# Kernel tuning notes

Hardware: AMD Instinct MI355X
Metric: run time of the kernel (lower is better)

Reference implementation:

```python
import jax, jax.numpy as jnp
import numpy as np

TEMPERATURE = 30.0
NUM_KERNELS = 4


def setup_inputs() -> dict:
    key = jax.random.key(0)
    ks = jax.random.split(key, 7)
    B, H, W, C = 32, 56, 56, 256
    F, KH, KW, K = 256, 3, 3, NUM_KERNELS
    hidden = C // 4  # attention_reduction_ratio = 4
    x = jax.random.normal(ks[0], (B, H, W, C), dtype=jnp.float32)
    # K parallel conv kernels (HWIO layout) and biases
    fan = KH * KW * C
    kernels = jax.random.normal(ks[1], (K, KH, KW, C, F), dtype=jnp.float32) / np.sqrt(fan)
    biases = jnp.zeros((K, F), dtype=jnp.float32)
    # attention MLP: GAP -> Dense(C//4, relu) -> Dense(K)
    w1 = jax.random.normal(ks[2], (C, hidden), dtype=jnp.float32) / np.sqrt(C)
    b1 = jnp.zeros((hidden,), dtype=jnp.float32)
    w2 = jax.random.normal(ks[3], (hidden, K), dtype=jnp.float32) / np.sqrt(hidden)
    b2 = jnp.zeros((K,), dtype=jnp.float32)
    return {"x": x, "kernels": kernels, "biases": biases,
            "w1": w1, "b1": b1, "w2": w2, "b2": b2}


def reference(x, kernels, biases, w1, b1, w2, b2):
    # Attention router: GAP -> Dense(relu) -> Dense(K) -> softmax(logits / tau)
    pooled = jnp.mean(x, axis=(1, 2))                       # [B, C]
    h = jax.nn.relu(pooled @ w1 + b1)                       # [B, C//4]
    logits = h @ w2 + b2                                    # [B, K]
    attn = jax.nn.softmax(logits / TEMPERATURE, axis=-1)    # [B, K]

    # K parallel conv branches (stride 1, SAME padding, dilation 1, groups 1)
    def conv_k(w, b):
        y = jax.lax.conv_general_dilated(
            x, w, window_strides=(1, 1), padding='SAME',
            dimension_numbers=('NHWC', 'HWIO', 'NHWC'))
        return y + b                                        # [B, H, W, F]

    ys = jax.vmap(conv_k)(kernels, biases)                  # [K, B, H, W, F]
    # per-sample weighted aggregation of branch outputs
    out = jnp.einsum('kbhwf,bk->bhwf', ys, attn)            # [B, H, W, F]
    return out
```

## Files before the change

kernel.cpp:

```cpp
#include <hip/hip_runtime.h>
#include <hip/hip_bf16.h>
#include <stdint.h>

typedef __bf16 bf16_t;
typedef __bf16 bf16x4 __attribute__((ext_vector_type(4)));
typedef __bf16 bf16x8 __attribute__((ext_vector_type(8)));
typedef float floatx4 __attribute__((ext_vector_type(4)));

#define B_ 32
#define HP 58
#define WP 66

#define XPAD_OFF   0u
#define WAGG_OFF   62717952u
#define POOLED_OFF 100466688u
#define ATTN_OFF   100499456u
#define BIASAGG_OFF 100499968u

__device__ __forceinline__ void async_copy16(const void* gsrc, void* ldst) {
  __builtin_amdgcn_global_load_lds(
      (const __attribute__((address_space(1))) unsigned int*)gsrc,
      (__attribute__((address_space(3))) unsigned int*)ldst, 16, 0, 0);
}

__global__ __launch_bounds__(256)
void pad_pool(const float* __restrict__ x, bf16_t* __restrict__ xpad,
              float* __restrict__ pooled) {
  const int hp = blockIdx.x;
  const int b  = blockIdx.y;
  const int t  = threadIdx.x;
  const int c4 = (t & 63) << 2;
  const int wq = t >> 6;
  const int h  = hp - 1;
  const bool hvalid = (h >= 0) && (h < 56);
  bf16_t* dst = xpad + ((size_t)(b * 58 + hp)) * (66 * 256);
  const float* srcrow = x + ((size_t)(b * 56 + (hvalid ? h : 0))) * (56 * 256);
  floatx4 sum = {0.f, 0.f, 0.f, 0.f};
  for (int wp = wq; wp < 66; wp += 4) {
    const int w = wp - 1;
    floatx4 v = {0.f, 0.f, 0.f, 0.f};
    if (hvalid && (unsigned)w < 56u) {
      v = *(const floatx4*)(srcrow + w * 256 + c4);
      sum += v;
    }
    bf16x4 r;
#pragma unroll
    for (int j = 0; j < 4; ++j) r[j] = (bf16_t)v[j];
    *(bf16x4*)(dst + wp * 256 + c4) = r;
  }
  __shared__ floatx4 red[4][64];
  red[wq][t & 63] = sum;
  __syncthreads();
  if (hvalid && t < 64) {
    floatx4 s = red[0][t] + red[1][t] + red[2][t] + red[3][t];
#pragma unroll
    for (int j = 0; j < 4; ++j) atomicAdd(&pooled[b * 256 + t * 4 + j], s[j]);
  }
}

__global__ __launch_bounds__(256)
void router(const float* __restrict__ pooled, const float* __restrict__ w1,
            const float* __restrict__ b1, const float* __restrict__ w2,
            const float* __restrict__ b2, const float* __restrict__ biases,
            float* __restrict__ attn, float* __restrict__ biasagg) {
  __shared__ float ps[8192];
  __shared__ float w1s[16384];
  __shared__ float hs[2048];
  __shared__ float lg[128];
  __shared__ float at[128];
  const int t = threadIdx.x;
  for (int i = t; i < 8192; i += 256) ps[i] = pooled[i] * (1.0f / 3136.0f);
  for (int i = t; i < 4096; i += 256)
    *(floatx4*)&w1s[i * 4] = *(const floatx4*)&w1[i * 4];
  __syncthreads();
  for (int task = t; task < 2048; task += 256) {
    const int b = task >> 6, j = task & 63;
    const float* pb = ps + b * 256;
    float s0 = 0.f, s1 = 0.f, s2 = 0.f, s3 = 0.f;
#pragma unroll 4
    for (int c = 0; c < 256; c += 4) {
      s0 += pb[c]     * w1s[c * 64 + j];
      s1 += pb[c + 1] * w1s[(c + 1) * 64 + j];
      s2 += pb[c + 2] * w1s[(c + 2) * 64 + j];
      s3 += pb[c + 3] * w1s[(c + 3) * 64 + j];
    }
    hs[task] = fmaxf((s0 + s1) + (s2 + s3) + b1[j], 0.f);
  }
  __syncthreads();
  if (t < 128) {
    int b = t >> 2, k = t & 3;
    float s = b2[k];
    const float* hb = hs + b * 64;
#pragma unroll 4
    for (int j = 0; j < 64; ++j) s += hb[j] * w2[j * 4 + k];
    lg[t] = s * (1.0f / 30.0f);
  }
  __syncthreads();
  if (t < 32) {
    int b = t;
    float z0 = lg[b*4], z1 = lg[b*4+1], z2 = lg[b*4+2], z3 = lg[b*4+3];
    float m = fmaxf(fmaxf(z0, z1), fmaxf(z2, z3));
    float e0 = expf(z0-m), e1 = expf(z1-m), e2 = expf(z2-m), e3 = expf(z3-m);
    float inv = 1.0f / (e0 + e1 + e2 + e3);
    at[b*4] = e0*inv; at[b*4+1] = e1*inv; at[b*4+2] = e2*inv; at[b*4+3] = e3*inv;
    attn[b*4] = at[b*4]; attn[b*4+1] = at[b*4+1];
    attn[b*4+2] = at[b*4+2]; attn[b*4+3] = at[b*4+3];
  }
  __syncthreads();
  for (int i = t; i < 8192; i += 256) {
    int b = i >> 8, f = i & 255;
    biasagg[i] = at[b*4]*biases[f] + at[b*4+1]*biases[256+f]
               + at[b*4+2]*biases[512+f] + at[b*4+3]*biases[768+f];
  }
}

__global__ __launch_bounds__(256)
void wagg_kernel(const float* __restrict__ kers, const float* __restrict__ attn,
                 bf16_t* __restrict__ wagg) {
  const int lid = blockIdx.x;
  const int xcd = lid & 7;
  const int sl  = lid >> 3;
  const int c8  = sl & 7;
  const int tap = sl >> 3;
  const int b0  = xcd << 2;
  const int t   = threadIdx.x;
  __shared__ bf16_t tile[4][32 * 260];

  float a[4][4];
#pragma unroll
  for (int i = 0; i < 4; ++i)
#pragma unroll
    for (int k = 0; k < 4; ++k) a[i][k] = attn[(b0 + i) * 4 + k];

  const float* k0 = kers + ((size_t)(0 * 9 + tap)) * 65536 + (size_t)(c8 * 32) * 256;
  const float* k1 = kers + ((size_t)(1 * 9 + tap)) * 65536 + (size_t)(c8 * 32) * 256;
  const float* k2 = kers + ((size_t)(2 * 9 + tap)) * 65536 + (size_t)(c8 * 32) * 256;
  const float* k3 = kers + ((size_t)(3 * 9 + tap)) * 65536 + (size_t)(c8 * 32) * 256;

  const int fq = t & 63;
  const int cl = t >> 6;
  const int f0 = fq * 4;
#pragma unroll
  for (int pass = 0; pass < 8; ++pass) {
    const int c_local = pass * 4 + cl;
    const size_t o = (size_t)c_local * 256 + f0;
    floatx4 v0 = *(const floatx4*)(k0 + o);
    floatx4 v1 = *(const floatx4*)(k1 + o);
    floatx4 v2 = *(const floatx4*)(k2 + o);
    floatx4 v3 = *(const floatx4*)(k3 + o);
#pragma unroll
    for (int i = 0; i < 4; ++i) {
      bf16x4 r;
#pragma unroll
      for (int j = 0; j < 4; ++j)
        r[j] = (bf16_t)(a[i][0] * v0[j] + a[i][1] * v1[j] + a[i][2] * v2[j] + a[i][3] * v3[j]);
      *(bf16x4*)&tile[i][c_local * 260 + f0] = r;
    }
  }
  __syncthreads();

#pragma unroll
  for (int i = 0; i < 4; ++i) {
    bf16_t* wt = wagg + ((size_t)((b0 + i) * 9 + tap)) * 65536 + c8 * 32;
#pragma unroll
    for (int pass = 0; pass < 4; ++pass) {
      const int gi = pass * 256 + t;
      const int f  = gi >> 2;
      const int cg = gi & 3;
      bf16x8 v;
#pragma unroll
      for (int jj = 0; jj < 8; ++jj) v[jj] = tile[i][(cg * 8 + jj) * 260 + f];
      *(bf16x8*)(wt + (size_t)f * 256 + cg * 8) = v;
    }
  }
}

#define PBUF_BYTES 40960
#define BBUF_BYTES 32768

__global__ __launch_bounds__(512, 2)
void conv_mfma(const bf16_t* __restrict__ xpad, const bf16_t* __restrict__ wagg,
               const float* __restrict__ biasagg, float* __restrict__ out) {
  __shared__ char lds[PBUF_BYTES + 3 * BBUF_BYTES];
  char* ldsP = lds;
  char* ldsB = lds + PBUF_BYTES;

  const int lid  = blockIdx.y * 14 + blockIdx.x;
  const int nid  = (lid & 7) * 56 + (lid >> 3);
  const int b    = nid / 14;
  const int tile = nid - b * 14;
  const int h0 = (tile >> 1) * 8;
  const int w0 = (tile & 1) * 28;

  const int tid  = threadIdx.x;
  const int lane = tid & 63;
  const int wv   = tid >> 6;
  const int mg   = wv >> 2;
  const int fs   = wv & 3;
  const int l15  = lane & 15;
  const int quad = lane >> 4;
  const int n0   = fs * 64;

  const char* xb = (const char*)xpad + (size_t)b * (HP * WP * 256 * 2);
  const char* wb = (const char*)wagg + (size_t)b * (9 * 256 * 256 * 2);

  int offs[7];
#pragma unroll
  for (int mi = 0; mi < 7; ++mi) {
    int m = mg * 112 + mi * 16 + l15;
    int ty = m / 28;
    int tx = m - ty * 28;
    offs[mi] = ty * 32 + tx;
  }
  int boff[4];
#pragma unroll
  for (int ni = 0; ni < 4; ++ni) {
    int f = n0 + ni * 16 + l15;
    boff[ni] = f * 128 + ((quad ^ (f & 7)) << 4);
  }
  int sb_off[4];
#pragma unroll
  for (int ii = 0; ii < 4; ++ii) {
    int i32 = wv * 4 + ii;
    int f = i32 * 8 + (lane >> 3);
    int gsrc = (lane & 7) ^ (f & 7);
    sb_off[ii] = f * 512 + gsrc * 16;
  }
  int sp_off[5];
#pragma unroll
  for (int ii = 0; ii < 5; ++ii) {
    int i40 = wv * 5 + ii;
    int p = i40 * 8 + (lane >> 3);
    int row = p >> 5, col = p & 31;
    int gsrc = (lane & 7) ^ (p & 7);
    sp_off[ii] = ((h0 + row) * WP + (w0 + col)) * 512 + gsrc * 16;
  }

  floatx4 acc[7][4];
#pragma unroll
  for (int mi = 0; mi < 7; ++mi)
#pragma unroll
    for (int ni = 0; ni < 4; ++ni) acc[mi][ni] = (floatx4){0.f, 0.f, 0.f, 0.f};

  auto stage_patch = [&](int cq) {
#pragma unroll
    for (int ii = 0; ii < 5; ++ii)
      async_copy16(xb + cq * 128 + sp_off[ii], ldsP + (wv * 5 + ii) * 1024);
  };
  auto stage_b = [&](int tap, int cq, int slot) {
    const char* wtb = wb + (size_t)tap * 131072 + cq * 128;
#pragma unroll
    for (int ii = 0; ii < 4; ++ii)
      async_copy16(wtb + sb_off[ii], ldsB + slot * BBUF_BYTES + (wv * 4 + ii) * 1024);
  };

  stage_patch(0);
  stage_b(0, 0, 0);

  bf16x8 aA[7], aB[7];
  int aoff[7];
  int slot = 0;

#pragma unroll 1
  for (int d = 0; d < 36; ++d) {
    const int cq  = d / 9;
    const int tap = d - cq * 9;
    const int s1 = (slot == 2) ? 0 : slot + 1;
    const bool last = (d == 35);

    if (!last) {
      const int nt = (tap == 8) ? 0 : tap + 1;
      const int nc = (tap == 8) ? cq + 1 : cq;
      stage_b(nt, nc, s1);
      asm volatile("s_waitcnt vmcnt(4)" ::: "memory");
    } else {
      asm volatile("s_waitcnt vmcnt(0)" ::: "memory");
    }
    __builtin_amdgcn_s_barrier();
    __builtin_amdgcn_sched_barrier(0);

    const char* bc = ldsB + slot * BBUF_BYTES;
    bf16x8 bv0 = *(const bf16x8*)(bc + boff[0]);
    bf16x8 bv1 = *(const bf16x8*)(bc + boff[1]);
    bf16x8 bv2 = *(const bf16x8*)(bc + boff[2]);
    bf16x8 bv3 = *(const bf16x8*)(bc + boff[3]);
    if (tap == 0) {
#pragma unroll
      for (int mi = 0; mi < 7; ++mi) {
        int p = offs[mi];
        aoff[mi] = (p << 7) + ((quad ^ (p & 7)) << 4);
        aA[mi] = *(const bf16x8*)(ldsP + aoff[mi]);
      }
    }
    __builtin_amdgcn_s_setprio(1);
#pragma unroll
    for (int mi = 0; mi < 7; ++mi) {
      acc[mi][0] = __builtin_amdgcn_mfma_f32_16x16x32_bf16(aA[mi], bv0, acc[mi][0], 0, 0, 0);
      acc[mi][1] = __builtin_amdgcn_mfma_f32_16x16x32_bf16(aA[mi], bv1, acc[mi][1], 0, 0, 0);
      acc[mi][2] = __builtin_amdgcn_mfma_f32_16x16x32_bf16(aA[mi], bv2, acc[mi][2], 0, 0, 0);
      acc[mi][3] = __builtin_amdgcn_mfma_f32_16x16x32_bf16(aA[mi], bv3, acc[mi][3], 0, 0, 0);
    }
    __builtin_amdgcn_s_setprio(0);

    bf16x8 cv0 = *(const bf16x8*)(bc + (boff[0] ^ 64));
    bf16x8 cv1 = *(const bf16x8*)(bc + (boff[1] ^ 64));
    bf16x8 cv2 = *(const bf16x8*)(bc + (boff[2] ^ 64));
    bf16x8 cv3 = *(const bf16x8*)(bc + (boff[3] ^ 64));
#pragma unroll
    for (int mi = 0; mi < 7; ++mi)
      aB[mi] = *(const bf16x8*)(ldsP + (aoff[mi] ^ 64));
    if (tap < 8) {
      const int ntapoff = ((tap + 1) / 3) * 32 + ((tap + 1) % 3);
#pragma unroll
      for (int mi = 0; mi < 7; ++mi) {
        int p = offs[mi] + ntapoff;
        aoff[mi] = (p << 7) + ((quad ^ (p & 7)) << 4);
        aA[mi] = *(const bf16x8*)(ldsP + aoff[mi]);
      }
    }
    __builtin_amdgcn_s_setprio(1);
#pragma unroll
    for (int mi = 0; mi < 7; ++mi) {
      acc[mi][0] = __builtin_amdgcn_mfma_f32_16x16x32_bf16(aB[mi], cv0, acc[mi][0], 0, 0, 0);
      acc[mi][1] = __builtin_amdgcn_mfma_f32_16x16x32_bf16(aB[mi], cv1, acc[mi][1], 0, 0, 0);
      acc[mi][2] = __builtin_amdgcn_mfma_f32_16x16x32_bf16(aB[mi], cv2, acc[mi][2], 0, 0, 0);
      acc[mi][3] = __builtin_amdgcn_mfma_f32_16x16x32_bf16(aB[mi], cv3, acc[mi][3], 0, 0, 0);
    }
    __builtin_amdgcn_s_setprio(0);

    if (tap == 8 && cq < 3) {
      __builtin_amdgcn_s_barrier();
      stage_patch(cq + 1);
    }
    slot = s1;
  }

  float bias[4];
#pragma unroll
  for (int ni = 0; ni < 4; ++ni) bias[ni] = biasagg[b * 256 + n0 + ni * 16 + l15];
  float* outb = out + (size_t)b * (56 * 56 * 256);
#pragma unroll
  for (int mi = 0; mi < 7; ++mi) {
#pragma unroll
    for (int rg = 0; rg < 4; ++rg) {
      int m = mg * 112 + mi * 16 + quad * 4 + rg;
      int ty = m / 28, tx = m - ty * 28;
      float* orow = outb + ((size_t)((h0 + ty) * 56) + (w0 + tx)) * 256 + n0 + l15;
#pragma unroll
      for (int ni = 0; ni < 4; ++ni) orow[ni * 16] = acc[mi][ni][rg] + bias[ni];
    }
  }
}

extern "C" void kernel_launch(void* const* d_in, const int* in_sizes, int n_in,
                              void* d_out, int out_size, void* d_ws, size_t ws_size,
                              hipStream_t stream) {
  const float* x      = (const float*)d_in[0];
  const float* kers   = (const float*)d_in[1];
  const float* biases = (const float*)d_in[2];
  const float* w1     = (const float*)d_in[3];
  const float* b1     = (const float*)d_in[4];
  const float* w2     = (const float*)d_in[5];
  const float* b2     = (const float*)d_in[6];
  float* outp = (float*)d_out;
  char* ws = (char*)d_ws;

  bf16_t* xpad   = (bf16_t*)(ws + XPAD_OFF);
  bf16_t* wagg   = (bf16_t*)(ws + WAGG_OFF);
  float* pooled  = (float*)(ws + POOLED_OFF);
  float* attn    = (float*)(ws + ATTN_OFF);
  float* biasagg = (float*)(ws + BIASAGG_OFF);

  hipMemsetAsync(pooled, 0, 32 * 256 * sizeof(float), stream);
  pad_pool<<<dim3(58, 32), 256, 0, stream>>>(x, xpad, pooled);
  router<<<1, 256, 0, stream>>>(pooled, w1, b1, w2, b2, biases, attn, biasagg);
  wagg_kernel<<<dim3(576), 256, 0, stream>>>(kers, attn, wagg);
  conv_mfma<<<dim3(14, 32), 512, 0, stream>>>(xpad, wagg, biasagg, outp);
}
```

Baseline: 361.8 us.

## Double-buffer input patch in LDS and move to two-slot weight pipeline

Gives the input patch its own two LDS buffers. The next channel quarter's patch is now prefetched early (at tap 0) instead of after a barrier at the end of each quarter, so the tap-8 to tap-0 transition no longer stalls on a fresh patch load. The weight ring drops from three slots to two, and each iteration ends with a full vmcnt(0) wait. A-fragment loads for the next step are issued across the loop boundary, and the second-half B and A fragment reads are hoisted ahead of the first MFMA group. The shallower weight prefetch and per-iteration full wait may expose more global-load latency in exchange for fewer patch stalls and one fewer barrier per quarter.

Measured after the change: 357.0 us. Within noise of the previous version (-1.3%).

```diff
diff --git a/kernel.cpp b/kernel.cpp
--- a/kernel.cpp
+++ b/kernel.cpp
@@ -181,9 +181,10 @@
 __global__ __launch_bounds__(512, 2)
 void conv_mfma(const bf16_t* __restrict__ xpad, const bf16_t* __restrict__ wagg,
                const float* __restrict__ biasagg, float* __restrict__ out) {
-  __shared__ char lds[PBUF_BYTES + 3 * BBUF_BYTES];
-  char* ldsP = lds;
-  char* ldsB = lds + PBUF_BYTES;
+  __shared__ char lds[2 * PBUF_BYTES + 2 * BBUF_BYTES];
+  char* ldsP0 = lds;
+  char* ldsP1 = lds + PBUF_BYTES;
+  char* ldsB  = lds + 2 * PBUF_BYTES;
 
   const int lid  = blockIdx.y * 14 + blockIdx.x;
   const int nid  = (lid & 7) * 56 + (lid >> 3);
@@ -242,10 +243,10 @@
 #pragma unroll
     for (int ni = 0; ni < 4; ++ni) acc[mi][ni] = (floatx4){0.f, 0.f, 0.f, 0.f};
 
-  auto stage_patch = [&](int cq) {
+  auto stage_patch = [&](int cq, char* pdst) {
 #pragma unroll
     for (int ii = 0; ii < 5; ++ii)
-      async_copy16(xb + cq * 128 + sp_off[ii], ldsP + (wv * 5 + ii) * 1024);
+      async_copy16(xb + cq * 128 + sp_off[ii], pdst + (wv * 5 + ii) * 1024);
   };
   auto stage_b = [&](int tap, int cq, int slot) {
     const char* wtb = wb + (size_t)tap * 131072 + cq * 128;
@@ -254,44 +255,52 @@
       async_copy16(wtb + sb_off[ii], ldsB + slot * BBUF_BYTES + (wv * 4 + ii) * 1024);
   };
 
-  stage_patch(0);
+  stage_patch(0, ldsP0);
   stage_b(0, 0, 0);
+  asm volatile("s_waitcnt vmcnt(0)" ::: "memory");
+  __builtin_amdgcn_s_barrier();
+  __builtin_amdgcn_sched_barrier(0);
 
   bf16x8 aA[7], aB[7];
   int aoff[7];
-  int slot = 0;
+#pragma unroll
+  for (int mi = 0; mi < 7; ++mi) {
+    int p = offs[mi];
+    aoff[mi] = (p << 7) + ((quad ^ (p & 7)) << 4);
+    aA[mi] = *(const bf16x8*)(ldsP0 + aoff[mi]);
+  }
 
 #pragma unroll 1
   for (int d = 0; d < 36; ++d) {
     const int cq  = d / 9;
     const int tap = d - cq * 9;
-    const int s1 = (slot == 2) ? 0 : slot + 1;
-    const bool last = (d == 35);
-
-    if (!last) {
+    const int cs  = cq & 1;
+    char* pbc = cs ? ldsP1 : ldsP0;
+    char* pbn = cs ? ldsP0 : ldsP1;
+    const char* bc = ldsB + (d & 1) * BBUF_BYTES;
+    const bool haveNext = (d < 35);
+
+    __builtin_amdgcn_s_barrier();
+    __builtin_amdgcn_sched_barrier(0);
+
+    if (haveNext) {
       const int nt = (tap == 8) ? 0 : tap + 1;
       const int nc = (tap == 8) ? cq + 1 : cq;
-      stage_b(nt, nc, s1);
-      asm volatile("s_waitcnt vmcnt(4)" ::: "memory");
-    } else {
-      asm volatile("s_waitcnt vmcnt(0)" ::: "memory");
-    }
-    __builtin_amdgcn_s_barrier();
-    __builtin_amdgcn_sched_barrier(0);
-
-    const char* bc = ldsB + slot * BBUF_BYTES;
+      stage_b(nt, nc, (d + 1) & 1);
+    }
+
     bf16x8 bv0 = *(const bf16x8*)(bc + boff[0]);
     bf16x8 bv1 = *(const bf16x8*)(bc + boff[1]);
     bf16x8 bv2 = *(const bf16x8*)(bc + boff[2]);
     bf16x8 bv3 = *(const bf16x8*)(bc + boff[3]);
-    if (tap == 0) {
-#pragma unroll
-      for (int mi = 0; mi < 7; ++mi) {
-        int p = offs[mi];
-        aoff[mi] = (p << 7) + ((quad ^ (p & 7)) << 4);
-        aA[mi] = *(const bf16x8*)(ldsP + aoff[mi]);
-      }
-    }
+    bf16x8 cv0 = *(const bf16x8*)(bc + (boff[0] ^ 64));
+    bf16x8 cv1 = *(const bf16x8*)(bc + (boff[1] ^ 64));
+    bf16x8 cv2 = *(const bf16x8*)(bc + (boff[2] ^ 64));
+    bf16x8 cv3 = *(const bf16x8*)(bc + (boff[3] ^ 64));
+#pragma unroll
+    for (int mi = 0; mi < 7; ++mi)
+      aB[mi] = *(const bf16x8*)(pbc + (aoff[mi] ^ 64));
+
     __builtin_amdgcn_s_setprio(1);
 #pragma unroll
     for (int mi = 0; mi < 7; ++mi) {
@@ -302,22 +311,18 @@
     }
     __builtin_amdgcn_s_setprio(0);
 
-    bf16x8 cv0 = *(const bf16x8*)(bc + (boff[0] ^ 64));
-    bf16x8 cv1 = *(const bf16x8*)(bc + (boff[1] ^ 64));
-    bf16x8 cv2 = *(const bf16x8*)(bc + (boff[2] ^ 64));
-    bf16x8 cv3 = *(const bf16x8*)(bc + (boff[3] ^ 64));
-#pragma unroll
-    for (int mi = 0; mi < 7; ++mi)
-      aB[mi] = *(const bf16x8*)(ldsP + (aoff[mi] ^ 64));
-    if (tap < 8) {
-      const int ntapoff = ((tap + 1) / 3) * 32 + ((tap + 1) % 3);
+    if (haveNext) {
+      const char* npb = (tap == 8) ? pbn : pbc;
+      const int ntapoff = (tap == 8) ? 0 : (((tap + 1) / 3) * 32 + ((tap + 1) % 3));
 #pragma unroll
       for (int mi = 0; mi < 7; ++mi) {
         int p = offs[mi] + ntapoff;
         aoff[mi] = (p << 7) + ((quad ^ (p & 7)) << 4);
-        aA[mi] = *(const bf16x8*)(ldsP + aoff[mi]);
+        aA[mi] = *(const bf16x8*)(npb + aoff[mi]);
       }
-    }
+      if (tap == 0 && cq < 3) stage_patch(cq + 1, pbn);
+    }
+
     __builtin_amdgcn_s_setprio(1);
 #pragma unroll
     for (int mi = 0; mi < 7; ++mi) {
@@ -328,11 +333,7 @@
     }
     __builtin_amdgcn_s_setprio(0);
 
-    if (tap == 8 && cq < 3) {
-      __builtin_amdgcn_s_barrier();
-      stage_patch(cq + 1);
-    }
-    slot = s1;
+    if (haveNext) asm volatile("s_waitcnt vmcnt(0)" ::: "memory");
   }
 
   float bias[4];
```
